# Kernel optimization log

Measured on AMD Instinct MI355X. Metric: run time of the kernel, lower is better.

## Reference

```python
import jax, jax.numpy as jnp
import numpy as np

B, S, D = 4, 4096, 1024

def setup_inputs() -> dict:
    key = jax.random.key(0)
    k1, k2, k3 = jax.random.split(key, 3)
    x = jax.random.normal(k1, (B, S, D), dtype=jnp.float32)
    # learned scalar decay logit; original initializes to 0.9 then sigmoids it
    decay_param = jnp.float32(0.9)
    # gate weight [D, D]; original inits to zeros (identity module) -- use small
    # random values so the baseline exercises the full math path
    W_gate = jax.random.normal(k3, (D, D), dtype=jnp.float32) * 0.02
    return {"x": x, "decay_param": decay_param, "W_gate": W_gate}

def reference(x, decay_param, W_gate):
    # x: [B, S, D]
    d = jax.nn.sigmoid(decay_param)  # scalar

    def step(state, x_t):
        # state, x_t: [B, D]
        new = d * state + (1.0 - d) * x_t
        return new, new

    x_t_first = jnp.swapaxes(x, 0, 1)  # [S, B, D]
    init = jnp.zeros((x.shape[0], x.shape[2]), dtype=x.dtype)
    _, causal = jax.lax.scan(step, init, x_t_first)  # [S, B, D]
    causal = jnp.swapaxes(causal, 0, 1)  # [B, S, D]
    # nn.Linear(D, D, bias=False): y = causal @ W^T
    return x + jnp.einsum('bsd,ed->bse', causal, W_gate)
```

## Files before the change

kernel.cpp:

```cpp
#include <hip/hip_runtime.h>
#include <hip/hip_bf16.h>

#define B_DIM 4
#define S_DIM 4096
#define D_DIM 1024
#define M_TOT (B_DIM * S_DIM)
#define LOOKBACK 32
#define CHUNK 128
#define NT2 (D_DIM / 32)

typedef unsigned short us;
typedef __attribute__((ext_vector_type(8))) short bf16x8;
typedef __attribute__((ext_vector_type(4))) float f32x4;
typedef __attribute__((ext_vector_type(4))) unsigned short u16x4;

__device__ __forceinline__ us f2bf(float f) {
  unsigned int u = __builtin_bit_cast(unsigned int, f);
  u += 0x7fffu + ((u >> 16) & 1u);
  return (us)(u >> 16);
}

__global__ __launch_bounds__(256) void scan_kernel(
    const float* __restrict__ x, const float* __restrict__ dp,
    us* __restrict__ causal) {
  const float dcy = 1.0f / (1.0f + expf(-dp[0]));
  const float omd = 1.0f - dcy;
  const int d0 = blockIdx.x * 512 + threadIdx.x;
  const int s0 = blockIdx.y * CHUNK;
  const size_t base = (size_t)blockIdx.z * S_DIM * D_DIM + d0;
  float st0 = 0.f, st1 = 0.f;
  if (s0 > 0) {
    const float* px = x + base + (size_t)(s0 - LOOKBACK) * D_DIM;
#pragma unroll 8
    for (int i = 0; i < LOOKBACK; ++i) {
      st0 = dcy * st0 + omd * px[0];
      st1 = dcy * st1 + omd * px[256];
      px += D_DIM;
    }
  }
  const float* px = x + base + (size_t)s0 * D_DIM;
  us* pc = causal + base + (size_t)s0 * D_DIM;
#pragma unroll 8
  for (int i = 0; i < CHUNK; ++i) {
    st0 = dcy * st0 + omd * px[0];
    st1 = dcy * st1 + omd * px[256];
    pc[0]   = f2bf(st0);
    pc[256] = f2bf(st1);
    px += D_DIM;
    pc += D_DIM;
  }
}

__global__ __launch_bounds__(256) void convw_kernel(
    const float* __restrict__ W, us* __restrict__ Wb) {
  const int i = (blockIdx.x * 256 + threadIdx.x) * 4;
  const float4 v = *(const float4*)(W + i);
  u16x4 o;
  o.x = f2bf(v.x); o.y = f2bf(v.y); o.z = f2bf(v.z); o.w = f2bf(v.w);
  *(u16x4*)(Wb + i) = o;
}

__global__ __launch_bounds__(256, 4) void gemm_kernel(
    const us* __restrict__ A,
    const us* __restrict__ Bw,
    const float* __restrict__ x,
    float* __restrict__ out) {
  __shared__ us smem_s[16384];

  const int bid = blockIdx.x;
  const int xcd = bid & 7;
  const int q = bid >> 3;
  const int m0 = (xcd * 16 + (q >> 3)) * 128;
  const int n0 = (q & 7) * 128;

  const int tid = threadIdx.x;
  const int lane = tid & 63;
  const int wave = tid >> 6;
  const int wr = wave >> 1;
  const int wc = wave & 1;
  const int lrow = lane & 15;
  const int ls   = lane >> 4;
  const int kx = (ls ^ (lrow & 3)) * 8;
  const int arow = (wr * 64 + lrow) * 32;
  const int brow = (wc * 64 + lrow) * 32;

  f32x4 acc[4][4];
#pragma unroll
  for (int i = 0; i < 4; ++i)
#pragma unroll
    for (int j = 0; j < 4; ++j) acc[i][j] = (f32x4)0.f;

#define STAGE(t, p)                                                            \
  {                                                                            \
    _Pragma("unroll")                                                          \
    for (int it = 0; it < 2; ++it) {                                           \
      const int c = it * 256 + tid;                                \
      const int r = c >> 2;                                        \
      const int slot = (c & 3) ^ (r & 3);                                      \
      __builtin_amdgcn_global_load_lds(                                        \
          (const __attribute__((address_space(1))) void*)(A +                  \
              (size_t)(m0 + r) * D_DIM + (t) * 32 + slot * 8),                 \
          (__attribute__((address_space(3))) void*)(smem_s + (p) * 8192 + c * 8),\
          16, 0, 0);                                                           \
      __builtin_amdgcn_global_load_lds(                                        \
          (const __attribute__((address_space(1))) void*)(Bw +                 \
              (size_t)(n0 + r) * D_DIM + (t) * 32 + slot * 8),                 \
          (__attribute__((address_space(3))) void*)(smem_s + (p) * 8192 +      \
              4096 + c * 8),                                                   \
          16, 0, 0);                                                           \
    }                                                                          \
  }

  STAGE(0, 0);
  STAGE(1, 1);
  asm volatile("s_waitcnt vmcnt(4)" ::: "memory");
  __builtin_amdgcn_s_barrier();

  for (int t = 0; t < NT2; ++t) {
    const int p = t & 1;
    const us* Ab = smem_s + p * 8192;
    const us* Bb = Ab + 4096;

    bf16x8 a[4], b[4];
#pragma unroll
    for (int mi = 0; mi < 4; ++mi)
      a[mi] = *(const bf16x8*)(Ab + arow + mi * 512 + kx);
#pragma unroll
    for (int nj = 0; nj < 4; ++nj)
      b[nj] = *(const bf16x8*)(Bb + brow + nj * 512 + kx);

    __builtin_amdgcn_s_setprio(1);
#pragma unroll
    for (int mi = 0; mi < 4; ++mi)
#pragma unroll
      for (int nj = 0; nj < 4; ++nj)
        acc[mi][nj] = __builtin_amdgcn_mfma_f32_16x16x32_bf16(
            a[mi], b[nj], acc[mi][nj], 0, 0, 0);
    __builtin_amdgcn_s_setprio(0);

    asm volatile("s_waitcnt vmcnt(0)" ::: "memory");
    __builtin_amdgcn_s_barrier();
    if (t + 2 < NT2) STAGE(t + 2, p);
  }

#pragma unroll
  for (int mi = 0; mi < 4; ++mi)
#pragma unroll
    for (int nj = 0; nj < 4; ++nj) {
      const int ocol = n0 + wc * 64 + nj * 16 + lrow;
      const int orow0 = m0 + wr * 64 + mi * 16 + ls * 4;
#pragma unroll
      for (int r = 0; r < 4; ++r) {
        const size_t idx = (size_t)(orow0 + r) * D_DIM + ocol;
        out[idx] = x[idx] + acc[mi][nj][r];
      }
    }
#undef STAGE
}

extern "C" void kernel_launch(void* const* d_in, const int* in_sizes, int n_in,
                              void* d_out, int out_size, void* d_ws, size_t ws_size,
                              hipStream_t stream) {
  const float* x  = (const float*)d_in[0];
  const float* dp = (const float*)d_in[1];
  const float* W  = (const float*)d_in[2];
  float* out = (float*)d_out;

  us* causal = (us*)d_ws;
  us* Wb = (us*)((char*)d_ws + (size_t)M_TOT * D_DIM * 2);

  dim3 g_scan(D_DIM / 512, S_DIM / CHUNK, B_DIM);
  scan_kernel<<<g_scan, 256, 0, stream>>>(x, dp, causal);

  convw_kernel<<<(D_DIM * D_DIM) / (256 * 4), 256, 0, stream>>>(W, Wb);

  gemm_kernel<<<(M_TOT / 128) * (D_DIM / 128), 256, 0, stream>>>(
      causal, Wb, x, out);
}
```

Measured before the change: 76.52 us.

## Double K-tile to 64 in GEMM and restructure prefetch with split LDS buffers

The GEMM K-step grows from 32 to 64, halving the main-loop iterations and barriers, with an 8-slot XOR swizzle in LDS. A is double-buffered while B uses a single buffer. The next tile is issued mid-iteration after a barrier once the B fragments and first half of A are in registers. LDS grows to 48KB and launch bounds drop to 3 blocks per CU, trading occupancy for more MFMA work per sync.

```diff
diff --git a/kernel.cpp b/kernel.cpp
--- a/kernel.cpp
+++ b/kernel.cpp
@@ -7,7 +7,7 @@
 #define M_TOT (B_DIM * S_DIM)
 #define LOOKBACK 32
 #define CHUNK 128
-#define NT2 (D_DIM / 32)
+#define NT (D_DIM / 64)
 
 typedef unsigned short us;
 typedef __attribute__((ext_vector_type(8))) short bf16x8;
@@ -60,12 +60,12 @@
   *(u16x4*)(Wb + i) = o;
 }
 
-__global__ __launch_bounds__(256, 4) void gemm_kernel(
+__global__ __launch_bounds__(256, 3) void gemm_kernel(
     const us* __restrict__ A,
     const us* __restrict__ Bw,
     const float* __restrict__ x,
     float* __restrict__ out) {
-  __shared__ us smem_s[16384];
+  __shared__ us smem_s[24576];
 
   const int bid = blockIdx.x;
   const int xcd = bid & 7;
@@ -80,9 +80,10 @@
   const int wc = wave & 1;
   const int lrow = lane & 15;
   const int ls   = lane >> 4;
-  const int kx = (ls ^ (lrow & 3)) * 8;
-  const int arow = (wr * 64 + lrow) * 32;
-  const int brow = (wc * 64 + lrow) * 32;
+  const int koff0 = ((0 + ls) ^ (lane & 7)) * 8;
+  const int koff1 = ((4 + ls) ^ (lane & 7)) * 8;
+  const int arow = (wr * 64 + lrow) * 64;
+  const int brow = (wc * 64 + lrow) * 64;
 
   f32x4 acc[4][4];
 #pragma unroll
@@ -90,44 +91,51 @@
 #pragma unroll
     for (int j = 0; j < 4; ++j) acc[i][j] = (f32x4)0.f;
 
-#define STAGE(t, p)                                                            \
+#define STAGE(SRC, rowbase, t, ldsbase)                                        \
   {                                                                            \
     _Pragma("unroll")                                                          \
-    for (int it = 0; it < 2; ++it) {                                           \
-      const int c = it * 256 + tid;                                \
-      const int r = c >> 2;                                        \
-      const int slot = (c & 3) ^ (r & 3);                                      \
+    for (int it = 0; it < 4; ++it) {                                           \
+      const int c = it * 256 + tid;                               \
+      const int r = c >> 3;                                       \
+      const int slot = (c & 7) ^ (r & 7);                                      \
       __builtin_amdgcn_global_load_lds(                                        \
-          (const __attribute__((address_space(1))) void*)(A +                  \
-              (size_t)(m0 + r) * D_DIM + (t) * 32 + slot * 8),                 \
-          (__attribute__((address_space(3))) void*)(smem_s + (p) * 8192 + c * 8),\
-          16, 0, 0);                                                           \
-      __builtin_amdgcn_global_load_lds(                                        \
-          (const __attribute__((address_space(1))) void*)(Bw +                 \
-              (size_t)(n0 + r) * D_DIM + (t) * 32 + slot * 8),                 \
-          (__attribute__((address_space(3))) void*)(smem_s + (p) * 8192 +      \
-              4096 + c * 8),                                                   \
+          (const __attribute__((address_space(1))) void*)((SRC) +              \
+              (size_t)((rowbase) + r) * D_DIM + (t) * 64 + slot * 8),          \
+          (__attribute__((address_space(3))) void*)(smem_s + (ldsbase) + c * 8),\
           16, 0, 0);                                                           \
     }                                                                          \
   }
 
-  STAGE(0, 0);
-  STAGE(1, 1);
-  asm volatile("s_waitcnt vmcnt(4)" ::: "memory");
+  STAGE(A,  m0, 0, 0);
+  STAGE(Bw, n0, 0, 16384);
+  asm volatile("s_waitcnt vmcnt(0)" ::: "memory");
   __builtin_amdgcn_s_barrier();
 
-  for (int t = 0; t < NT2; ++t) {
+  for (int t = 0; t < NT; ++t) {
     const int p = t & 1;
     const us* Ab = smem_s + p * 8192;
-    const us* Bb = Ab + 4096;
+    const us* Bb = smem_s + 16384;
 
-    bf16x8 a[4], b[4];
+    bf16x8 b[4][2], a0[4], a1[4];
+#pragma unroll
+    for (int nj = 0; nj < 4; ++nj) {
+      b[nj][0] = *(const bf16x8*)(Bb + brow + nj * 1024 + koff0);
+      b[nj][1] = *(const bf16x8*)(Bb + brow + nj * 1024 + koff1);
+    }
 #pragma unroll
     for (int mi = 0; mi < 4; ++mi)
-      a[mi] = *(const bf16x8*)(Ab + arow + mi * 512 + kx);
+      a0[mi] = *(const bf16x8*)(Ab + arow + mi * 1024 + koff0);
+
+    __builtin_amdgcn_s_barrier();
+
+    if (t + 1 < NT) {
+      STAGE(Bw, n0, t + 1, 16384);
+      STAGE(A,  m0, t + 1, (p ^ 1) * 8192);
+    }
+
 #pragma unroll
-    for (int nj = 0; nj < 4; ++nj)
-      b[nj] = *(const bf16x8*)(Bb + brow + nj * 512 + kx);
+    for (int mi = 0; mi < 4; ++mi)
+      a1[mi] = *(const bf16x8*)(Ab + arow + mi * 1024 + koff1);
 
     __builtin_amdgcn_s_setprio(1);
 #pragma unroll
@@ -135,12 +143,17 @@
 #pragma unroll
       for (int nj = 0; nj < 4; ++nj)
         acc[mi][nj] = __builtin_amdgcn_mfma_f32_16x16x32_bf16(
-            a[mi], b[nj], acc[mi][nj], 0, 0, 0);
+            a0[mi], b[nj][0], acc[mi][nj], 0, 0, 0);
+#pragma unroll
+    for (int mi = 0; mi < 4; ++mi)
+#pragma unroll
+      for (int nj = 0; nj < 4; ++nj)
+        acc[mi][nj] = __builtin_amdgcn_mfma_f32_16x16x32_bf16(
+            a1[mi], b[nj][1], acc[mi][nj], 0, 0, 0);
     __builtin_amdgcn_s_setprio(0);
 
     asm volatile("s_waitcnt vmcnt(0)" ::: "memory");
     __builtin_amdgcn_s_barrier();
-    if (t + 2 < NT2) STAGE(t + 2, p);
   }
 
 #pragma unroll
```

New measurement: 70.20 us. 1.09x faster.
